# Kernel tuning notes

Measured on AMD Instinct MI355X. Metric: run time of the kernel, lower is better.

## Reference

```python
import jax, jax.numpy as jnp
import numpy as np

NUM_HEADS = 8
NUM_KV_HEADS = 2
PATCH = 16
STRIDE = 8
HORIZON = 96
NQ = 3
EPS_RMS = 1e-6
EPS_REVIN = 1e-5


def rms_norm(x, scale):
    return x * jax.lax.rsqrt(jnp.mean(x * x, axis=-1, keepdims=True) + EPS_RMS) * scale


def lstm_scan(xs, wi, wh, b):
    # xs: (N, T, Din); flax OptimizedLSTMCell gate order i, f, g, o
    N = xs.shape[0]
    H = wh.shape[0]

    def step(carry, x_t):
        c, h = carry
        z = x_t @ wi + h @ wh + b
        i, f, g, o = jnp.split(z, 4, axis=-1)
        c = jax.nn.sigmoid(f) * c + jax.nn.sigmoid(i) * jnp.tanh(g)
        h = jax.nn.sigmoid(o) * jnp.tanh(c)
        return (c, h), h

    init = (jnp.zeros((N, H), xs.dtype), jnp.zeros((N, H), xs.dtype))
    _, hs = jax.lax.scan(step, init, jnp.swapaxes(xs, 0, 1))
    return jnp.swapaxes(hs, 0, 1)  # (N, T, H)


def gqa(x, wq, wk, wv, wo):
    # x: (B, S, D); non-causal grouped-query attention
    B, S, D = x.shape
    hd = wq.shape[1] // NUM_HEADS
    q = (x @ wq).reshape(B, S, NUM_HEADS, hd)
    k = (x @ wk).reshape(B, S, NUM_KV_HEADS, hd)
    v = (x @ wv).reshape(B, S, NUM_KV_HEADS, hd)
    rep = NUM_HEADS // NUM_KV_HEADS
    k = jnp.repeat(k, rep, axis=2)
    v = jnp.repeat(v, rep, axis=2)
    scale = jnp.asarray(1.0 / np.sqrt(hd), x.dtype)
    attn = jax.nn.softmax(jnp.einsum('bqhd,bkhd->bhqk', q, k) * scale, axis=-1)
    out = jnp.einsum('bhqk,bkhd->bqhd', attn, v).reshape(B, S, NUM_HEADS * hd)
    return out @ wo, attn


def setup_inputs() -> dict:
    key = jax.random.key(0)
    ks = jax.random.split(key, 12)
    b, d, m, T = 8, 16, 8, 512
    H, H2 = 256, 512
    NB = 4

    def w(k, shape, fan_in):
        return jax.random.normal(k, shape, jnp.float32) / np.sqrt(fan_in)

    return {
        'series': jax.random.normal(ks[0], (b, d, m, T), jnp.float32),
        'revin_scale': jnp.ones((m,), jnp.float32),
        'revin_bias': jnp.zeros((m,), jnp.float32),
        'up_w': w(ks[1], (PATCH, H), PATCH),
        'lstm_wi': w(ks[2], (NB, H, 4 * H2), H),
        'lstm_wh': w(ks[3], (NB, H2, 4 * H2), H2),
        'lstm_b': jnp.zeros((NB, 4 * H2), jnp.float32),
        'norm_scale': jnp.ones((NB, H2), jnp.float32),
        'wq': w(ks[4], (NB, H2, H2), H2),
        'wk': w(ks[5], (NB, H2, H2 // 4), H2),
        'wv': w(ks[6], (NB, H2, H2 // 4), H2),
        'wo': w(ks[7], (NB, H2, H2), H2),
        'down_w': w(ks[8], (NB, H2, H), H2),
        'head_norm_scale': jnp.ones((H,), jnp.float32),
        'point_w': w(ks[9], (H, HORIZON), H),
        'quant_w': w(ks[10], (H, HORIZON * NQ), H),
    }


def reference(series, revin_scale, revin_bias, up_w, lstm_wi, lstm_wh, lstm_b,
              norm_scale, wq, wk, wv, wo, down_w, head_norm_scale, point_w, quant_w):
    b, d, m, T = series.shape
    num_blocks = lstm_wi.shape[0]
    H = up_w.shape[1]
    H2 = lstm_wh.shape[1]

    # RevIN instance norm over time with per-metric affine
    mean = series.mean(axis=-1, keepdims=True)
    std = jnp.sqrt(series.var(axis=-1, keepdims=True) + EPS_REVIN)
    sc = revin_scale[:, None]
    bi = revin_bias[:, None]
    normed = (series - mean) / std * sc + bi

    # Patcher (seq_len=512, patch=16, stride=8 -> 63 patches, no padding needed)
    n_p = (T - PATCH) // STRIDE + 1
    idx = jnp.arange(n_p)[:, None] * STRIDE + jnp.arange(PATCH)
    patches = normed[..., idx]            # (b, d, m, np, ps)
    x = patches @ up_w                    # (b, d, m, np, H)

    for blk in range(num_blocks):
        s = x.reshape(b * d * m, n_p, H)
        hs = lstm_scan(s, lstm_wi[blk], lstm_wh[blk], lstm_b[blk])  # (bdm, np, H2)
        # '(b d m) np h -> (b m np) d h'
        hs = hs.reshape(b, d, m, n_p, H2).transpose(0, 2, 3, 1, 4).reshape(b * m * n_p, d, H2)
        nrm = rms_norm(hs, norm_scale[blk])
        mix, _ = gqa(nrm, wq[blk], wk[blk], wv[blk], wo[blk])
        bel = mix @ down_w[blk]           # (bmnp, d, H)
        # '(b m np) d h -> b d m np h'
        x = bel.reshape(b, m, n_p, d, H).transpose(0, 3, 1, 2, 4)

    # pooling_mode == 'last' with device mixer: last block's belief at last patch
    last = x[:, :, :, -1, :]              # (b, d, m, H)
    nb = rms_norm(last, head_norm_scale)
    point = nb @ point_w                  # (b, d, m, horizon)
    quant = (nb @ quant_w).reshape(b, d, m, HORIZON, NQ).transpose(4, 0, 1, 2, 3)

    def denorm(y):
        return (y - bi) / sc * std + mean

    point_u = denorm(point)
    quant_u = denorm(quant)               # broadcasts over leading quantile axis
    return jnp.concatenate([point_u[None], quant_u], axis=0)  # (1+NQ, b, d, m, horizon)
```

## Files before the change

kernel.cpp:

```cpp
#include <hip/hip_runtime.h>
#include <hip/hip_bf16.h>

#define NP 63

typedef __attribute__((ext_vector_type(8))) short short8;
typedef __attribute__((ext_vector_type(4))) float f32x4;
typedef __attribute__((ext_vector_type(4))) int i32x4;
typedef unsigned char uchar;

__device__ __forceinline__ float sigf(float x){ return 1.0f/(1.0f+expf(-x)); }
__device__ __forceinline__ float u2f(ushort u){ __hip_bfloat16 h; *(ushort*)&h = u; return __bfloat162float(h); }
__device__ __forceinline__ ushort f2u(float f){ __hip_bfloat16 h = __float2bfloat16(f); return *(ushort*)&h; }

__device__ __forceinline__ float fexp2(float x){ float r; asm("v_exp_f32 %0, %1" : "=v"(r) : "v"(x)); return r; }
__device__ __forceinline__ float frcp (float x){ float r; asm("v_rcp_f32 %0, %1" : "=v"(r) : "v"(x)); return r; }
#define LOG2E 1.442695040888963f
__device__ __forceinline__ float sig_fast(float x){
  float a = fminf(fmaxf(-LOG2E*x, -126.f), 126.f);
  return frcp(1.f + fexp2(a));
}
__device__ __forceinline__ float tanh_fast(float x){
  float a = fminf(fmaxf(-2.f*LOG2E*x, -126.f), 126.f);
  float e = fexp2(a);
  return (1.f - e) * frcp(1.f + e);
}

__global__ void __launch_bounds__(256) k_revin(const float* __restrict__ series,
    float* __restrict__ meanv, float* __restrict__ stdv, int* __restrict__ bar)
{
  int n = blockIdx.x, tid = threadIdx.x;
  if(n==0 && tid<64) bar[tid] = 0;
  __shared__ float s1[256], s2[256];
  const float* p = series + n*512;
  float a = 0.f, b = 0.f;
  for(int t=tid;t<512;t+=256){ float v=p[t]; a+=v; b+=v*v; }
  s1[tid]=a; s2[tid]=b; __syncthreads();
  for(int s=128;s>0;s>>=1){
    if(tid<s){ s1[tid]+=s1[tid+s]; s2[tid]+=s2[tid+s]; }
    __syncthreads();
  }
  if(tid==0){
    float mu = s1[0]*(1.f/512.f);
    float var = fmaxf(s2[0]*(1.f/512.f) - mu*mu, 0.f);
    meanv[n]=mu; stdv[n]=sqrtf(var+1e-5f);
  }
}

__global__ void __launch_bounds__(256) k_patch(const float* __restrict__ series,
    const float* __restrict__ rs, const float* __restrict__ rb,
    const float* __restrict__ up_w, const float* __restrict__ meanv,
    const float* __restrict__ stdv, ushort* __restrict__ x)
{
  int n = blockIdx.x, tid = threadIdx.x;
  int m = n & 7;
  __shared__ float sn[512];
  float mu = meanv[n], sd = stdv[n];
  float A = rs[m]/sd, C = rb[m] - mu*A;
  const float* p = series + n*512;
  for(int t=tid;t<512;t+=256) sn[t] = p[t]*A + C;
  __syncthreads();
  float w[16];
  #pragma unroll
  for(int i=0;i<16;i++) w[i] = up_w[i*256+tid];
  ushort* xo = x + n*(NP*256);
  for(int pi=0;pi<NP;pi++){
    float acc=0.f;
    #pragma unroll
    for(int i=0;i<16;i++) acc = fmaf(sn[pi*8+i], w[i], acc);
    xo[pi*256+tid] = f2u(acc);
  }
}

__global__ void __launch_bounds__(256) k_wod(const float* __restrict__ wo,
    const float* __restrict__ dw, float* __restrict__ wod)
{
  int i = blockIdx.x, blk = blockIdx.y, tid = threadIdx.x;
  __shared__ float row[512];
  const float* wr = wo + (blk*512 + i)*512;
  for(int k=tid;k<512;k+=256) row[k]=wr[k];
  __syncthreads();
  const float* d = dw + blk*512*256;
  float acc=0.f;
  for(int k=0;k<512;k++) acc = fmaf(row[k], d[k*256+tid], acc);
  wod[(blk*512+i)*256+tid]=acc;
}

__global__ void __launch_bounds__(256) k_tr_wodt(const float* __restrict__ wod, ushort* __restrict__ wodt)
{
  __shared__ float tile[32][33];
  int blk = blockIdx.z;
  int n0 = blockIdx.x*32, k0 = blockIdx.y*32;
  int tid = threadIdx.x;
  #pragma unroll
  for(int i=0;i<4;i++){
    int idx = tid + 256*i; int kl = idx>>5, nl = idx&31;
    tile[kl][nl] = wod[blk*512*256 + (k0+kl)*256 + n0+nl];
  }
  __syncthreads();
  #pragma unroll
  for(int i=0;i<4;i++){
    int idx = tid + 256*i; int nl = idx>>5, kl = idx&31;
    wodt[blk*256*512 + (n0+nl)*512 + k0+kl] = f2u(tile[kl][nl]);
  }
}

__global__ void __launch_bounds__(256) k_tr_lstmw(const float* __restrict__ wi,
    const float* __restrict__ wh, ushort* __restrict__ wt)
{
  __shared__ float tile[32][33];
  int blk = blockIdx.z;
  int n0 = blockIdx.x*32, k0 = blockIdx.y*32;
  int tid = threadIdx.x;
  #pragma unroll
  for(int i=0;i<4;i++){
    int idx = tid + 256*i; int kl = idx>>5, nl = idx&31;
    int k = k0+kl, n = n0+nl;
    float v = (k<256) ? wi[blk*256*2048 + k*2048 + n]
                      : wh[blk*512*2048 + (k-256)*2048 + n];
    tile[kl][nl] = v;
  }
  __syncthreads();
  #pragma unroll
  for(int i=0;i<4;i++){
    int idx = tid + 256*i; int nl = idx>>5, kl = idx&31;
    wt[blk*2048*768 + (n0+nl)*768 + k0+kl] = f2u(tile[kl][nl]);
  }
}

__global__ void __launch_bounds__(256) k_tr_qkvw(const float* __restrict__ wq,
    const float* __restrict__ wk, const float* __restrict__ wv,
    const float* __restrict__ ns, ushort* __restrict__ wqkvt)
{
  __shared__ float tile[32][33];
  int blk = blockIdx.z;
  int n0 = blockIdx.x*32, k0 = blockIdx.y*32;
  int tid = threadIdx.x;
  #pragma unroll
  for(int i=0;i<4;i++){
    int idx = tid + 256*i; int kl = idx>>5, nl = idx&31;
    int k = k0+kl, n = n0+nl;
    float v;
    if(n < 512)      v = wq[blk*512*512 + k*512 + n];
    else if(n < 640) v = wk[blk*512*128 + k*128 + (n-512)];
    else             v = wv[blk*512*128 + k*128 + (n-640)];
    tile[kl][nl] = v * ns[blk*512 + k];
  }
  __syncthreads();
  #pragma unroll
  for(int i=0;i<4;i++){
    int idx = tid + 256*i; int nl = idx>>5, kl = idx&31;
    wqkvt[blk*768*512 + (n0+nl)*512 + k0+kl] = f2u(tile[kl][nl]);
  }
}

__global__ void __launch_bounds__(256,1) k_lstm_scan(
    const ushort* __restrict__ x, ushort* __restrict__ hs,
    const ushort* __restrict__ wt, const float* __restrict__ bias,
    uchar* __restrict__ flags, int tagbase)
{
  __shared__ __align__(16) short Bwh[128*512];
  __shared__ __align__(16) ushort hstage[64*32];
  int fb = blockIdx.x;
  int g = (fb & 7) | ((fb >> 4) & 8);
  int y = (fb >> 3) & 15;
  int n0 = g*64, jj0 = y*32;
  int tid = threadIdx.x;
  int wv = tid>>6, lane = tid&63, quad = lane>>4, l16 = lane&15;
  int wrow = wv>>1, wcol = wv&1;

  for(int i=tid; i<8192; i+=256){
    int c = i>>6, kb = i&63;
    short8 v = *(const short8*)(wt + ((c>>5)*512 + jj0 + (c&31))*768 + 256 + kb*8);
    *(short8*)((char*)Bwh + c*1024 + ((kb*16) ^ ((c&7)<<4))) = v;
  }
  int jj = jj0 + wcol*16 + l16;
  short8 bwi[4][8];
  #pragma unroll
  for(int gg=0; gg<4; gg++){
    const ushort* wp = wt + (gg*512 + jj)*768 + quad*8;
    #pragma unroll
    for(int ck=0; ck<8; ck++) bwi[gg][ck] = *(const short8*)(wp + ck*32);
  }
  float bI=bias[jj], bF=bias[512+jj], bG=bias[1024+jj], bO=bias[1536+jj];
  float cs[2][4];
  #pragma unroll
  for(int a=0;a<2;a++){
    #pragma unroll
    for(int r=0;r<4;r++) cs[a][r]=0.f;
  }
  const ushort* xb0 = x  + (n0 + wrow*32 + l16)*(NP*256) + quad*8;
  const ushort* hb0 = hs + (n0 + wrow*32 + l16)*(NP*512) + quad*8;
  int xorb = (l16&7)<<4;
  uchar* myflag = flags + g*16 + y;
  const uchar* gflags = flags + g*16;
  __syncthreads();

  for(int t=0; t<NP; ++t){
    f32x4 acc[4][2];
    #pragma unroll
    for(int gg=0; gg<4; gg++){ acc[gg][0]=(f32x4){0.f,0.f,0.f,0.f}; acc[gg][1]=(f32x4){0.f,0.f,0.f,0.f}; }

    #pragma unroll
    for(int ck=0; ck<8; ck++){
      short8 a0 = *(const short8*)(xb0 + t*256 + ck*32);
      short8 a1 = *(const short8*)(xb0 + 16*(NP*256) + t*256 + ck*32);
      #pragma unroll
      for(int gg=0; gg<4; gg++){
        acc[gg][0] = __builtin_amdgcn_mfma_f32_16x16x32_bf16(a0, bwi[gg][ck], acc[gg][0], 0,0,0);
        acc[gg][1] = __builtin_amdgcn_mfma_f32_16x16x32_bf16(a1, bwi[gg][ck], acc[gg][1], 0,0,0);
      }
    }

    if(t > 0){
      if(tid==0){
        uint tag = (uint)(tagbase + t);
        while(1){
          i32x4 f;
          asm volatile("global_load_dwordx4 %0, %1, off sc0 sc1\n\ts_waitcnt vmcnt(0)"
                       : "=&v"(f) : "v"(gflags) : "memory");
          uint ok = 1u;
          #pragma unroll
          for(int q=0;q<4;q++){
            uint w = (uint)f[q];
            if(( w      &0xffu) < tag) ok=0;
            if(((w>>8 ) &0xffu) < tag) ok=0;
            if(((w>>16) &0xffu) < tag) ok=0;
            if( (w>>24)         < tag) ok=0;
          }
          if(ok) break;
          __builtin_amdgcn_s_sleep(1);
        }
      }
      __syncthreads();

      const ushort* hb = hb0 + (t-1)*512;
      #pragma unroll
      for(int ck=0; ck<16; ck++){
        short8 a0 = *(const short8*)(hb + ck*32);
        short8 a1 = *(const short8*)(hb + 16*(NP*512) + ck*32);
        #pragma unroll
        for(int gg=0; gg<4; gg++){
          int c = gg*32 + wcol*16 + l16;
          short8 bh = *(short8*)((char*)Bwh + c*1024 + ((ck*64 + quad*16) ^ xorb));
          acc[gg][0] = __builtin_amdgcn_mfma_f32_16x16x32_bf16(a0, bh, acc[gg][0], 0,0,0);
          acc[gg][1] = __builtin_amdgcn_mfma_f32_16x16x32_bf16(a1, bh, acc[gg][1], 0,0,0);
        }
      }
    }

    #pragma unroll
    for(int a=0;a<2;a++){
      #pragma unroll
      for(int r=0;r<4;r++){
        int rowl = wrow*32 + a*16 + quad*4 + r;
        float zi=acc[0][a][r]+bI, zf=acc[1][a][r]+bF, zg=acc[2][a][r]+bG, zo=acc[3][a][r]+bO;
        float c = sig_fast(zf)*cs[a][r] + sig_fast(zi)*tanh_fast(zg);
        cs[a][r] = c;
        float hv = sig_fast(zo)*tanh_fast(c);
        int coll = wcol*16 + l16;
        int off = rowl*64 + ((coll*2) ^ (((rowl>>2)&3)<<4));
        *(ushort*)((char*)hstage + off) = f2u(hv);
      }
    }
    __syncthreads();
    {
      int rowl = tid>>2, c0b = (tid&3)*16;
      int off = rowl*64 + (c0b ^ (((rowl>>2)&3)<<4));
      i32x4 vv = *(const i32x4*)((const char*)hstage + off);
      ushort* gp = hs + ((size_t)(n0+rowl)*NP + t)*512 + jj0 + (tid&3)*8;
      asm volatile("global_store_dwordx4 %0, %1, off sc0 sc1" :: "v"(gp), "v"(vv) : "memory");
    }
    __syncthreads();
    if(tid==0 && t < NP-1){
      uint v = (uint)(tagbase + t + 1);
      asm volatile("global_store_byte %0, %1, off sc0 sc1" :: "v"(myflag), "v"(v) : "memory");
    }
  }
}

__global__ void __launch_bounds__(256) k_qkv_m(
    const ushort* __restrict__ hs, const ushort* __restrict__ wqkvt,
    ushort* __restrict__ qkv)
{
  __shared__ short As[128*40];
  __shared__ short Bs[128*40];
  __shared__ float rvs[128];
  int tid = threadIdx.x;
  int r0 = blockIdx.x*128, c0 = blockIdx.y*128;
  int wv = tid>>6, lane = tid&63, quad = lane>>4, l16 = lane&15;
  int wrow = wv>>1, wcol = wv&1;
  int arow0 = tid>>2, akp = tid&3;
  const ushort* aptr[2];
  #pragma unroll
  for(int i=0;i<2;i++){
    int r = r0 + arow0 + i*64;
    int bq = r/8064; int rr = r - bq*8064;
    int m = rr/1008; int rem = rr - m*1008;
    int p = rem>>4; int d = rem&15;
    int n = (bq*16+d)*8+m;
    aptr[i] = hs + (n*NP+p)*512 + akp*8;
  }
  f32x4 acc[4][4];
  #pragma unroll
  for(int b=0;b<4;b++){
    #pragma unroll
    for(int a=0;a<4;a++) acc[b][a] = (f32x4){0.f,0.f,0.f,0.f};
  }
  float ssq0 = 0.f, ssq1 = 0.f;
  for(int k0=0;k0<512;k0+=32){
    {
      short8 av = *(const short8*)(aptr[0] + k0);
      *(short8*)&As[arow0*40 + akp*8] = av;
      #pragma unroll
      for(int e=0;e<8;e++){ float vv = u2f((ushort)av[e]); ssq0 = fmaf(vv, vv, ssq0); }
    }
    {
      short8 av = *(const short8*)(aptr[1] + k0);
      *(short8*)&As[(arow0+64)*40 + akp*8] = av;
      #pragma unroll
      for(int e=0;e<8;e++){ float vv = u2f((ushort)av[e]); ssq1 = fmaf(vv, vv, ssq1); }
    }
    #pragma unroll
    for(int i=0;i<2;i++){
      int pc = tid + 256*i; int rl=pc>>2, kp=pc&3;
      *(short8*)&Bs[rl*40+kp*8] = *(const short8*)(wqkvt + (c0+rl)*512 + k0 + kp*8);
    }
    __syncthreads();
    short8 af[4], bfr[4];
    #pragma unroll
    for(int a=0;a<4;a++) af[a] = *(short8*)&As[(wrow*64 + a*16 + l16)*40 + quad*8];
    #pragma unroll
    for(int b=0;b<4;b++) bfr[b] = *(short8*)&Bs[(wcol*64 + b*16 + l16)*40 + quad*8];
    #pragma unroll
    for(int b=0;b<4;b++){
      #pragma unroll
      for(int a=0;a<4;a++)
        acc[b][a] = __builtin_amdgcn_mfma_f32_16x16x32_bf16(af[a], bfr[b], acc[b][a], 0,0,0);
    }
    __syncthreads();
  }
  ssq0 += __shfl_xor(ssq0, 1); ssq0 += __shfl_xor(ssq0, 2);
  ssq1 += __shfl_xor(ssq1, 1); ssq1 += __shfl_xor(ssq1, 2);
  if(akp==0){
    rvs[arow0]    = rsqrtf(ssq0*(1.f/512.f)+1e-6f);
    rvs[arow0+64] = rsqrtf(ssq1*(1.f/512.f)+1e-6f);
  }
  __syncthreads();
  #pragma unroll
  for(int a=0;a<4;a++){
    #pragma unroll
    for(int rg=0;rg<4;rg++){
      int rowl = wrow*64 + a*16 + quad*4 + rg;
      int rw = r0 + rowl;
      float rv = rvs[rowl];
      #pragma unroll
      for(int b=0;b<4;b++){
        int c = c0 + wcol*64 + b*16 + l16;
        qkv[rw*768 + c] = f2u(acc[b][a][rg] * rv);
      }
    }
  }
}

__global__ void __launch_bounds__(256) k_attn(ushort* __restrict__ qkv)
{
  int r3 = blockIdx.x, h = blockIdx.y;
  int tid = threadIdx.x;
  __shared__ float qs[16][64];
  __shared__ float ks[16][65];
  __shared__ float vs[16][64];
  __shared__ float P[16][17];
  ushort* base = qkv + r3*16*768;
  int xx = tid&63, s4 = tid>>6;
  int kvh = (h>>2)*64;
  #pragma unroll
  for(int a=0;a<4;a++){
    int s = s4 + 4*a;
    qs[s][xx] = u2f(base[s*768 + h*64 + xx]);
    ks[s][xx] = u2f(base[s*768 + 512 + kvh + xx]);
    vs[s][xx] = u2f(base[s*768 + 640 + kvh + xx]);
  }
  __syncthreads();
  int i = tid>>4, j = tid&15;
  float sc = 0.f;
  #pragma unroll
  for(int xq=0;xq<64;xq++) sc = fmaf(qs[i][xq], ks[j][xq], sc);
  P[i][j] = sc*0.125f;
  __syncthreads();
  float row[16];
  #pragma unroll
  for(int jj=0;jj<16;jj++) row[jj] = P[i][jj];
  float mx = row[0];
  #pragma unroll
  for(int jj=1;jj<16;jj++) mx = fmaxf(mx, row[jj]);
  float sum = 0.f;
  #pragma unroll
  for(int jj=0;jj<16;jj++) sum += expf(row[jj]-mx);
  float pme = expf(row[j]-mx)/sum;
  __syncthreads();
  P[i][j] = pme;
  __syncthreads();
  #pragma unroll
  for(int a=0;a<4;a++){
    int s = s4 + 4*a;
    float o = 0.f;
    #pragma unroll
    for(int jj=0;jj<16;jj++) o = fmaf(P[s][jj], vs[jj][xx], o);
    base[s*768 + h*64 + xx] = f2u(o);
  }
}

__global__ void __launch_bounds__(256) k_bel_m(
    const ushort* __restrict__ qkv, const ushort* __restrict__ wodt,
    ushort* __restrict__ x)
{
  __shared__ short As[128*40];
  __shared__ short Bs[128*40];
  int tid = threadIdx.x;
  int r0 = blockIdx.x*128, c0 = blockIdx.y*128;
  int wv = tid>>6, lane = tid&63, quad = lane>>4, l16 = lane&15;
  int wrow = wv>>1, wcol = wv&1;
  int arow0 = tid>>2, akp = tid&3;
  const ushort* aptr0 = qkv + (r0+arow0)*768 + akp*8;
  const ushort* aptr1 = qkv + (r0+arow0+64)*768 + akp*8;
  f32x4 acc[4][4];
  #pragma unroll
  for(int b=0;b<4;b++){
    #pragma unroll
    for(int a=0;a<4;a++) acc[b][a] = (f32x4){0.f,0.f,0.f,0.f};
  }
  for(int k0=0;k0<512;k0+=32){
    *(short8*)&As[arow0*40 + akp*8]      = *(const short8*)(aptr0 + k0);
    *(short8*)&As[(arow0+64)*40 + akp*8] = *(const short8*)(aptr1 + k0);
    #pragma unroll
    for(int i=0;i<2;i++){
      int pc = tid + 256*i; int rl=pc>>2, kp=pc&3;
      *(short8*)&Bs[rl*40+kp*8] = *(const short8*)(wodt + (c0+rl)*512 + k0 + kp*8);
    }
    __syncthreads();
    short8 af[4], bfr[4];
    #pragma unroll
    for(int a=0;a<4;a++) af[a] = *(short8*)&As[(wrow*64 + a*16 + l16)*40 + quad*8];
    #pragma unroll
    for(int b=0;b<4;b++) bfr[b] = *(short8*)&Bs[(wcol*64 + b*16 + l16)*40 + quad*8];
    #pragma unroll
    for(int b=0;b<4;b++){
      #pragma unroll
      for(int a=0;a<4;a++)
        acc[b][a] = __builtin_amdgcn_mfma_f32_16x16x32_bf16(af[a], bfr[b], acc[b][a], 0,0,0);
    }
    __syncthreads();
  }
  #pragma unroll
  for(int a=0;a<4;a++){
    #pragma unroll
    for(int rg=0;rg<4;rg++){
      int rw = r0 + wrow*64 + a*16 + quad*4 + rg;
      int bq = rw/8064; int rr = rw - bq*8064;
      int m = rr/1008; int rem = rr - m*1008;
      int p = rem>>4; int d = rem&15;
      int n = (bq*16+d)*8+m;
      ushort* xo = x + (n*NP+p)*256;
      #pragma unroll
      for(int b=0;b<4;b++){
        int c = c0 + wcol*64 + b*16 + l16;
        xo[c] = f2u(acc[b][a][rg]);
      }
    }
  }
}

__global__ void __launch_bounds__(256) k_head(const ushort* __restrict__ x,
    const float* __restrict__ meanv, const float* __restrict__ stdv,
    const float* __restrict__ rs, const float* __restrict__ rb,
    const float* __restrict__ hns, const float* __restrict__ pw,
    const float* __restrict__ qw, float* __restrict__ out)
{
  int n = blockIdx.x, tid = threadIdx.x;
  __shared__ float nb[256];
  __shared__ float red[256];
  float v = u2f(x[(n*NP + 62)*256 + tid]);
  red[tid] = v*v; __syncthreads();
  for(int s=128;s>0;s>>=1){
    if(tid<s) red[tid]+=red[tid+s];
    __syncthreads();
  }
  float rinv = rsqrtf(red[0]*(1.f/256.f)+1e-6f);
  nb[tid] = v*rinv*hns[tid];
  __syncthreads();
  int m = n&7;
  float mu=meanv[n], sd=stdv[n], sc=rs[m], bi=rb[m];
  for(int col=tid; col<384; col+=256){
    float acc=0.f;
    int slot, hh;
    if(col < 96){
      for(int k=0;k<256;k++) acc = fmaf(nb[k], pw[k*96+col], acc);
      slot = 0; hh = col;
    } else {
      int cq = col-96;
      for(int k=0;k<256;k++) acc = fmaf(nb[k], qw[k*288+cq], acc);
      int qi = cq - (cq/3)*3;
      slot = 1 + qi; hh = cq/3;
    }
    float y = (acc - bi)/sc*sd + mu;
    out[(slot*1024 + n)*96 + hh] = y;
  }
}

extern "C" void kernel_launch(void* const* d_in, const int* in_sizes, int n_in,
                              void* d_out, int out_size, void* d_ws, size_t ws_size,
                              hipStream_t stream)
{
  const float* series    = (const float*)d_in[0];
  const float* rs        = (const float*)d_in[1];
  const float* rb        = (const float*)d_in[2];
  const float* up_w      = (const float*)d_in[3];
  const float* lstm_wi   = (const float*)d_in[4];
  const float* lstm_wh   = (const float*)d_in[5];
  const float* lstm_b    = (const float*)d_in[6];
  const float* norm_scale= (const float*)d_in[7];
  const float* wq        = (const float*)d_in[8];
  const float* wk        = (const float*)d_in[9];
  const float* wv        = (const float*)d_in[10];
  const float* wo        = (const float*)d_in[11];
  const float* down_w    = (const float*)d_in[12];
  const float* head_ns   = (const float*)d_in[13];
  const float* point_w   = (const float*)d_in[14];
  const float* quant_w   = (const float*)d_in[15];
  float* out = (float*)d_out;

  float* ws = (float*)d_ws;
  float*  meanv = ws;
  float*  stdv  = meanv + 1024;
  float*  rmsi  = stdv  + 1024;
  float*  cst   = rmsi  + 64512;
  float*  wodf  = cst   + 524288;
  ushort* xbuf  = (ushort*)(wodf + 524288);
  ushort* hsb   = xbuf  + 16515072;
  ushort* qkvb  = hsb   + 33030144;
  ushort* wt    = qkvb  + 49545216;
  ushort* wqkvt = wt    + 6291456;
  ushort* wodt  = wqkvt + 1572864;
  int*    bar   = (int*)cst;

  k_revin<<<1024,256,0,stream>>>(series, meanv, stdv, bar);
  k_patch<<<1024,256,0,stream>>>(series, rs, rb, up_w, meanv, stdv, xbuf);
  k_wod<<<dim3(512,4),256,0,stream>>>(wo, down_w, wodf);
  k_tr_wodt<<<dim3(8,16,4),256,0,stream>>>(wodf, wodt);
  k_tr_lstmw<<<dim3(64,24,4),256,0,stream>>>(lstm_wi, lstm_wh, wt);
  k_tr_qkvw<<<dim3(24,16,4),256,0,stream>>>(wq, wk, wv, norm_scale, wqkvt);

  for(int blk=0; blk<4; blk++){
    const ushort* wt_b = wt + blk*2048*768;
    const float*  bb   = lstm_b + blk*2048;
    k_lstm_scan<<<256,256,0,stream>>>(xbuf, hsb, wt_b, bb, (uchar*)bar, blk*NP);
    k_qkv_m<<<dim3(504,6),256,0,stream>>>(hsb, wqkvt + blk*768*512, qkvb);
    k_attn<<<dim3(4032,8),256,0,stream>>>(qkvb);
    k_bel_m<<<dim3(504,2),256,0,stream>>>(qkvb, wodt + blk*256*512, xbuf);
  }
  k_head<<<1024,256,0,stream>>>(xbuf, meanv, stdv, rs, rb, head_ns, point_w, quant_w, out);
}
```

Baseline: 3.191 ms.

## Prefetch LSTM operand loads in a register ring and merge attention heads per block

In the LSTM scan, the x and h operand fragments are now loaded into a four-deep register ring and fetched four steps ahead of the MFMAs that use them. This is meant to hide global load latency behind the matrix ops on the serial recurrent path. The attention kernel now launches one block per 16-row group and loops over all 8 heads. It stages the whole 16x768 QKV tile in shared memory once, so the shared K/V rows are no longer re-read from global memory by each head. The cost is more registers in the scan, more shared memory and a serial head loop with extra barriers in attention, which lowers parallelism there.

Result: slower. 3.346 ms (+4.9%).

```diff
diff --git a/kernel.cpp b/kernel.cpp
--- a/kernel.cpp
+++ b/kernel.cpp
@@ -200,14 +200,28 @@
     #pragma unroll
     for(int gg=0; gg<4; gg++){ acc[gg][0]=(f32x4){0.f,0.f,0.f,0.f}; acc[gg][1]=(f32x4){0.f,0.f,0.f,0.f}; }
 
-    #pragma unroll
-    for(int ck=0; ck<8; ck++){
-      short8 a0 = *(const short8*)(xb0 + t*256 + ck*32);
-      short8 a1 = *(const short8*)(xb0 + 16*(NP*256) + t*256 + ck*32);
-      #pragma unroll
-      for(int gg=0; gg<4; gg++){
-        acc[gg][0] = __builtin_amdgcn_mfma_f32_16x16x32_bf16(a0, bwi[gg][ck], acc[gg][0], 0,0,0);
-        acc[gg][1] = __builtin_amdgcn_mfma_f32_16x16x32_bf16(a1, bwi[gg][ck], acc[gg][1], 0,0,0);
+    {
+      const ushort* xb  = xb0 + t*256;
+      const ushort* xb2 = xb + 16*(NP*256);
+      short8 v0[4], v1[4];
+      #pragma unroll
+      for(int p=0;p<4;p++){
+        v0[p] = *(const short8*)(xb  + p*32);
+        v1[p] = *(const short8*)(xb2 + p*32);
+      }
+      #pragma unroll
+      for(int ck=0; ck<8; ck++){
+        short8 a0 = v0[ck&3];
+        short8 a1 = v1[ck&3];
+        if(ck < 4){
+          v0[ck&3] = *(const short8*)(xb  + (ck+4)*32);
+          v1[ck&3] = *(const short8*)(xb2 + (ck+4)*32);
+        }
+        #pragma unroll
+        for(int gg=0; gg<4; gg++){
+          acc[gg][0] = __builtin_amdgcn_mfma_f32_16x16x32_bf16(a0, bwi[gg][ck], acc[gg][0], 0,0,0);
+          acc[gg][1] = __builtin_amdgcn_mfma_f32_16x16x32_bf16(a1, bwi[gg][ck], acc[gg][1], 0,0,0);
+        }
       }
     }
 
@@ -233,11 +247,22 @@
       }
       __syncthreads();
 
-      const ushort* hb = hb0 + (t-1)*512;
+      const ushort* hb  = hb0 + (t-1)*512;
+      const ushort* hb2 = hb + 16*(NP*512);
+      short8 w0[4], w1[4];
+      #pragma unroll
+      for(int p=0;p<4;p++){
+        w0[p] = *(const short8*)(hb  + p*32);
+        w1[p] = *(const short8*)(hb2 + p*32);
+      }
       #pragma unroll
       for(int ck=0; ck<16; ck++){
-        short8 a0 = *(const short8*)(hb + ck*32);
-        short8 a1 = *(const short8*)(hb + 16*(NP*512) + ck*32);
+        short8 a0 = w0[ck&3];
+        short8 a1 = w1[ck&3];
+        if(ck < 12){
+          w0[ck&3] = *(const short8*)(hb  + (ck+4)*32);
+          w1[ck&3] = *(const short8*)(hb2 + (ck+4)*32);
+        }
         #pragma unroll
         for(int gg=0; gg<4; gg++){
           int c = gg*32 + wcol*16 + l16;
@@ -364,49 +389,56 @@
 
 __global__ void __launch_bounds__(256) k_attn(ushort* __restrict__ qkv)
 {
-  int r3 = blockIdx.x, h = blockIdx.y;
-  int tid = threadIdx.x;
+  int r3 = blockIdx.x;
+  int tid = threadIdx.x;
+  __shared__ ushort qk[16*768];
   __shared__ float qs[16][64];
   __shared__ float ks[16][65];
   __shared__ float vs[16][64];
   __shared__ float P[16][17];
   ushort* base = qkv + r3*16*768;
+  for(int i=tid; i<1536; i+=256)
+    *(short8*)&qk[i*8] = *(const short8*)&base[i*8];
+  __syncthreads();
   int xx = tid&63, s4 = tid>>6;
-  int kvh = (h>>2)*64;
-  #pragma unroll
-  for(int a=0;a<4;a++){
-    int s = s4 + 4*a;
-    qs[s][xx] = u2f(base[s*768 + h*64 + xx]);
-    ks[s][xx] = u2f(base[s*768 + 512 + kvh + xx]);
-    vs[s][xx] = u2f(base[s*768 + 640 + kvh + xx]);
-  }
-  __syncthreads();
   int i = tid>>4, j = tid&15;
-  float sc = 0.f;
-  #pragma unroll
-  for(int xq=0;xq<64;xq++) sc = fmaf(qs[i][xq], ks[j][xq], sc);
-  P[i][j] = sc*0.125f;
-  __syncthreads();
-  float row[16];
-  #pragma unroll
-  for(int jj=0;jj<16;jj++) row[jj] = P[i][jj];
-  float mx = row[0];
-  #pragma unroll
-  for(int jj=1;jj<16;jj++) mx = fmaxf(mx, row[jj]);
-  float sum = 0.f;
-  #pragma unroll
-  for(int jj=0;jj<16;jj++) sum += expf(row[jj]-mx);
-  float pme = expf(row[j]-mx)/sum;
-  __syncthreads();
-  P[i][j] = pme;
-  __syncthreads();
-  #pragma unroll
-  for(int a=0;a<4;a++){
-    int s = s4 + 4*a;
-    float o = 0.f;
-    #pragma unroll
-    for(int jj=0;jj<16;jj++) o = fmaf(P[s][jj], vs[jj][xx], o);
-    base[s*768 + h*64 + xx] = f2u(o);
+  for(int h=0; h<8; h++){
+    int kvh = (h>>2)*64;
+    #pragma unroll
+    for(int a=0;a<4;a++){
+      int s = s4 + 4*a;
+      qs[s][xx] = u2f(qk[s*768 + h*64 + xx]);
+      ks[s][xx] = u2f(qk[s*768 + 512 + kvh + xx]);
+      vs[s][xx] = u2f(qk[s*768 + 640 + kvh + xx]);
+    }
+    __syncthreads();
+    float sc = 0.f;
+    #pragma unroll
+    for(int xq=0;xq<64;xq++) sc = fmaf(qs[i][xq], ks[j][xq], sc);
+    P[i][j] = sc*0.125f;
+    __syncthreads();
+    float row[16];
+    #pragma unroll
+    for(int jj=0;jj<16;jj++) row[jj] = P[i][jj];
+    float mx = row[0];
+    #pragma unroll
+    for(int jj=1;jj<16;jj++) mx = fmaxf(mx, row[jj]);
+    float sum = 0.f;
+    #pragma unroll
+    for(int jj=0;jj<16;jj++) sum += expf(row[jj]-mx);
+    float pme = expf(row[j]-mx)/sum;
+    __syncthreads();
+    P[i][j] = pme;
+    __syncthreads();
+    #pragma unroll
+    for(int a=0;a<4;a++){
+      int s = s4 + 4*a;
+      float o = 0.f;
+      #pragma unroll
+      for(int jj=0;jj<16;jj++) o = fmaf(P[s][jj], vs[jj][xx], o);
+      base[s*768 + h*64 + xx] = f2u(o);
+    }
+    __syncthreads();
   }
 }
 
@@ -555,7 +587,7 @@
     const float*  bb   = lstm_b + blk*2048;
     k_lstm_scan<<<256,256,0,stream>>>(xbuf, hsb, wt_b, bb, (uchar*)bar, blk*NP);
     k_qkv_m<<<dim3(504,6),256,0,stream>>>(hsb, wqkvt + blk*768*512, qkvb);
-    k_attn<<<dim3(4032,8),256,0,stream>>>(qkvb);
+    k_attn<<<4032,256,0,stream>>>(qkvb);
     k_bel_m<<<dim3(504,2),256,0,stream>>>(qkvb, wodt + blk*256*512, xbuf);
   }
   k_head<<<1024,256,0,stream>>>(xbuf, meanv, stdv, rs, rb, head_ns, point_w, quant_w, out);
```
